# Kernel tuning notes

Hardware: AMD Instinct MI355X
Metric: run time of the kernel (lower is better)

The kernel has to match this reference:

```python
import jax, jax.numpy as jnp
import numpy as np

LN_EPS = 1e-5


def setup_inputs() -> dict:
    key = jax.random.key(0)
    ks = jax.random.split(key, 5)
    N, E, D = 50000, 600000, 128
    x = jax.random.normal(ks[0], (N, D), dtype=jnp.float32)
    edge_index = jax.random.randint(ks[1], (2, E), 0, N, dtype=jnp.int64)
    W_l = jax.random.normal(ks[2], (D, D), dtype=jnp.float32) * (1.0 / np.sqrt(D))
    b_l = jnp.zeros((D,), dtype=jnp.float32)
    W_r = jax.random.normal(ks[3], (D, D), dtype=jnp.float32) * (1.0 / np.sqrt(D))
    gamma = jnp.ones((D,), dtype=jnp.float32)
    beta = jnp.zeros((D,), dtype=jnp.float32)
    return {"x": x, "edge_index": edge_index, "W_l": W_l, "b_l": b_l,
            "W_r": W_r, "gamma": gamma, "beta": beta}


def reference(x, edge_index, W_l, b_l, W_r, gamma, beta):
    # SAGEConv (mean aggregation): out = lin_l(mean_{j in N(i)} x_j) + lin_r(x_i)
    N = x.shape[0]
    src, dst = edge_index[0], edge_index[1]
    msg = x[src]                                                # (E, D) gather
    agg = jax.ops.segment_sum(msg, dst, num_segments=N)         # (N, D) scatter-add
    cnt = jax.ops.segment_sum(jnp.ones_like(dst, dtype=x.dtype), dst, num_segments=N)
    mean = agg / jnp.maximum(cnt, 1.0)[:, None]
    h = mean @ W_l.T + b_l + x @ W_r.T                          # (N, D)
    # LayerNorm over feature dim
    mu = jnp.mean(h, axis=-1, keepdims=True)
    var = jnp.mean(jnp.square(h - mu), axis=-1, keepdims=True)
    h = (h - mu) * jax.lax.rsqrt(var + LN_EPS) * gamma + beta
    # ReLU; Dropout is identity in eval mode
    return jax.nn.relu(h)
```

## Files before the change

### kernel.cpp

```cpp
#include <hip/hip_runtime.h>
#include <stdint.h>

#define DIM 128
#define LN_EPS 1e-5f
#define BROWS 32
#define BINB 256
#define NT1 1024
#define SCAP 8
#define NBKT_MAX 1600
#define LELLS 56
#define LOVF 64
#define OVFCAP 4096
#define ATS 264
#define PINIT ((int)0xAAAAAAAA)

typedef __attribute__((ext_vector_type(8))) short bf16x8;
typedef __attribute__((ext_vector_type(4))) float f32x4;

static __device__ __forceinline__ uint16_t f2bf(float f) {
    uint32_t u = __float_as_uint(f);
    return (uint16_t)((u + 0x7fffu + ((u >> 16) & 1u)) >> 16);
}
static __device__ __forceinline__ float bf_lo(uint32_t w) {
    return __uint_as_float(w << 16);
}
static __device__ __forceinline__ float bf_hi(uint32_t w) {
    return __uint_as_float(w & 0xffff0000u);
}

__global__ __launch_bounds__(NT1) void bin_kernel(
    const int* __restrict__ ei,
    const float* __restrict__ x,
    const float* __restrict__ Wl,
    const float* __restrict__ Wr,
    uint8_t* __restrict__ cnt, uint32_t* __restrict__ bedge,
    int* __restrict__ novf, int* __restrict__ ovf,
    uint16_t* __restrict__ x16, uint16_t* __restrict__ wc,
    int E, int N, int nbkt)
{
    __shared__ int hist[NBKT_MAX];
    const int t = threadIdx.x, b = blockIdx.x;

    for (int i = t; i < nbkt; i += NT1) hist[i] = 0;
    __syncthreads();

    const int chunk = (E + BINB - 1) / BINB;
    const int e0 = b * chunk;
    const int e1 = (e0 + chunk < E) ? e0 + chunk : E;

    for (int e = e0 + t; e < e1; e += NT1)
        atomicAdd(&hist[ei[E + e] >> 5], 1);
    __syncthreads();

    for (int i = t; i < nbkt; i += NT1) {
        int c = hist[i];
        cnt[(size_t)i * BINB + b] = (uint8_t)(c > 255 ? 255 : c);
        hist[i] = 0;
    }
    __syncthreads();

    for (int e = e0 + t; e < e1; e += NT1) {
        int src = ei[e];
        int dst = ei[E + e];
        int bkt = dst >> 5;
        int r = atomicAdd(&hist[bkt], 1);
        if (r < SCAP) {
            bedge[((size_t)bkt * BINB + b) * SCAP + r] =
                ((uint32_t)(dst & 31) << 27) | (uint32_t)src;
        } else {
            int q = atomicAdd(novf, 1) - PINIT;
            if (q >= 0 && q < OVFCAP) { ovf[2 * q] = dst; ovf[2 * q + 1] = src; }
        }
    }

    {
        int tid = b * NT1 + t, nth = BINB * NT1;
        int nxp = (N * DIM) >> 1;
        for (int i = tid; i < nxp; i += nth) {
            float2 v = *(const float2*)(x + 2 * i);
            uint32_t u = ((uint32_t)f2bf(v.y) << 16) | (uint32_t)f2bf(v.x);
            ((uint32_t*)x16)[i] = u;
        }
        for (int i = tid; i < DIM * 256; i += nth) {
            int d = i >> 8, k = i & 255;
            float v = (k < DIM) ? Wl[d * DIM + k] : Wr[d * DIM + (k - DIM)];
            wc[i] = f2bf(v);
        }
    }
}

__global__ __launch_bounds__(256, 4) void fused_kernel(
    const uint16_t* __restrict__ x16,
    const uint8_t* __restrict__ cnt,
    const uint32_t* __restrict__ bedge,
    const int* __restrict__ novf,
    const int* __restrict__ ovf,
    const uint16_t* __restrict__ wc,
    const float* __restrict__ bl,
    const float* __restrict__ gma,
    const float* __restrict__ bta,
    float* __restrict__ out,
    int N, int E)
{
    __shared__ int ell_s[BROWS][LELLS];
    __shared__ int cnt_s[BROWS];
    __shared__ int lovf_s[LOVF];
    __shared__ int nlovf_s;
    __shared__ uint16_t atile[2][16 * ATS];
    __shared__ float pln[2][16][2][2];

    const int t    = threadIdx.x;
    const int lane = t & 63;
    const int w    = t >> 6;
    const int p    = w >> 1;
    const int h    = w & 1;
    const int tile_row0 = blockIdx.x * BROWS + p * 16;
    const int grow0     = tile_row0 + h * 8;
    const int lb        = p * 16 + h * 8;

    if (t < BROWS) cnt_s[t] = 0;
    if (t == BROWS) nlovf_s = 0;
    __syncthreads();

    if (t < BINB) {
        int c = cnt[(size_t)blockIdx.x * BINB + t];
        c = (c < SCAP) ? c : SCAP;
        const uint32_t* sp = bedge + ((size_t)blockIdx.x * BINB + t) * SCAP;
        for (int r = 0; r < c; ++r) {
            uint32_t pk = sp[r];
            int local = pk >> 27;
            int rr = atomicAdd(&cnt_s[local], 1);
            if (rr < LELLS) ell_s[local][rr] = (int)(pk & 0x07FFFFFF);
            else {
                int q = atomicAdd(&nlovf_s, 1);
                if (q < LOVF) lovf_s[q] = (int)pk;
            }
        }
    }
    __syncthreads();

    int dgx[8], nell[8], mx = 0;
    #pragma unroll
    for (int r = 0; r < 8; ++r) {
        int d = __builtin_amdgcn_readfirstlane(cnt_s[lb + r]);
        dgx[r] = d;
        int tt = d < LELLS ? d : LELLS;
        nell[r] = tt;
        mx = (tt > mx) ? tt : mx;
    }

    int soff[8];
    #pragma unroll
    for (int r = 0; r < 8; ++r)
        soff[r] = (lane < nell[r]) ? (ell_s[lb + r][lane] << 8) : 0;

    float m0[8], m1[8];
    #pragma unroll
    for (int r = 0; r < 8; ++r) { m0[r] = 0.0f; m1[r] = 0.0f; }

    const char* xb = (const char*)x16;
    uint32_t u[8];
    #pragma unroll
    for (int r = 0; r < 8; ++r) {
        int o = __builtin_amdgcn_readlane(soff[r], 0);
        u[r] = *(const uint32_t*)(xb + (uint32_t)o + 4 * lane);
    }

    for (int j = 0; j < mx; ++j) {
        uint32_t un[8];
        int jn = (j + 1 < mx) ? j + 1 : j;
        #pragma unroll
        for (int r = 0; r < 8; ++r) {
            int o = __builtin_amdgcn_readlane(soff[r], jn);
            un[r] = *(const uint32_t*)(xb + (uint32_t)o + 4 * lane);
        }
        #pragma unroll
        for (int r = 0; r < 8; ++r) {
            float pr = (j < nell[r]) ? 1.0f : 0.0f;
            m0[r] = fmaf(pr, bf_lo(u[r]), m0[r]);
            m1[r] = fmaf(pr, bf_hi(u[r]), m1[r]);
            u[r] = un[r];
        }
    }

    {
        int nl = __builtin_amdgcn_readfirstlane(nlovf_s);
        nl = (nl < 0) ? 0 : (nl > LOVF ? LOVF : nl);
        for (int i = 0; i < nl; ++i) {
            uint32_t pk = (uint32_t)lovf_s[i];
            int local = pk >> 27;
            if (local >= lb && local < lb + 8) {
                int srco = (int)(pk & 0x07FFFFFF);
                uint32_t uu = *(const uint32_t*)(x16 + (size_t)srco * DIM + 2 * lane);
                float v0 = bf_lo(uu), v1 = bf_hi(uu);
                #pragma unroll
                for (int r = 0; r < 8; ++r) {
                    float pr = (local == lb + r) ? 1.0f : 0.0f;
                    m0[r] = fmaf(pr, v0, m0[r]);
                    m1[r] = fmaf(pr, v1, m1[r]);
                }
            }
        }
    }

    {
        int no = __builtin_amdgcn_readfirstlane(novf[0]) - PINIT;
        no = (no < 0) ? 0 : (no > OVFCAP ? OVFCAP : no);
        for (int i = 0; i < no; ++i) {
            int dsto = __builtin_amdgcn_readfirstlane(ovf[2 * i]);
            int srco = __builtin_amdgcn_readfirstlane(ovf[2 * i + 1]);
            if (dsto >= grow0 && dsto < grow0 + 8) {
                uint32_t uu = *(const uint32_t*)(x16 + (size_t)srco * DIM + 2 * lane);
                float v0 = bf_lo(uu), v1 = bf_hi(uu);
                #pragma unroll
                for (int r = 0; r < 8; ++r) {
                    bool hit = (dsto == grow0 + r);
                    float pr = hit ? 1.0f : 0.0f;
                    m0[r] = fmaf(pr, v0, m0[r]);
                    m1[r] = fmaf(pr, v1, m1[r]);
                    dgx[r] += hit ? 1 : 0;
                }
            }
        }
    }

    {
        uint16_t* at = atile[p];
        #pragma unroll
        for (int r = 0; r < 8; ++r) {
            int row = grow0 + r;
            int rr = (row < N) ? row : 0;
            float rc = (dgx[r] > 0) ? (1.0f / (float)dgx[r]) : 0.0f;
            int lr = h * 8 + r;
            ushort2 mu2;
            mu2.x = f2bf(m0[r] * rc);
            mu2.y = f2bf(m1[r] * rc);
            *(ushort2*)&at[lr * ATS + 2 * lane] = mu2;
            uint32_t xv = *(const uint32_t*)(x16 + (size_t)rr * DIM + 2 * lane);
            *(uint32_t*)&at[lr * ATS + 128 + 2 * lane] = xv;
        }
    }
    __syncthreads();

    const int nsub = lane & 15;
    const int quad = lane >> 4;
    const uint16_t* at = atile[p];

    f32x4 acc[4];
    #pragma unroll
    for (int tt = 0; tt < 4; ++tt) {
        float b = bl[(h * 4 + tt) * 16 + nsub];
        acc[tt] = (f32x4){b, b, b, b};
    }

    #pragma unroll
    for (int c = 0; c < 8; ++c) {
        bf16x8 af = *(const bf16x8*)&at[nsub * ATS + c * 32 + quad * 8];
        #pragma unroll
        for (int tt = 0; tt < 4; ++tt) {
            int tg = h * 4 + tt;
            bf16x8 bfr = *(const bf16x8*)&wc[(size_t)(tg * 16 + nsub) * 256 + c * 32 + quad * 8];
            acc[tt] = __builtin_amdgcn_mfma_f32_16x16x32_bf16(af, bfr, acc[tt], 0, 0, 0);
        }
    }

    #pragma unroll
    for (int i = 0; i < 4; ++i) {
        float s = 0.0f, q = 0.0f;
        #pragma unroll
        for (int tt = 0; tt < 4; ++tt) {
            float v = acc[tt][i];
            s += v;
            q += v * v;
        }
        #pragma unroll
        for (int off = 1; off < 16; off <<= 1) {
            s += __shfl_xor(s, off, 64);
            q += __shfl_xor(q, off, 64);
        }
        if (nsub == 0) {
            pln[p][quad * 4 + i][h][0] = s;
            pln[p][quad * 4 + i][h][1] = q;
        }
    }
    __syncthreads();

    #pragma unroll
    for (int i = 0; i < 4; ++i) {
        int lrow = quad * 4 + i;
        float s = pln[p][lrow][0][0] + pln[p][lrow][1][0];
        float q = pln[p][lrow][0][1] + pln[p][lrow][1][1];
        float mu = s * (1.0f / 128.0f);
        float var = q * (1.0f / 128.0f) - mu * mu;
        float rs = rsqrtf(fmaxf(var, 0.0f) + LN_EPS);
        int grow = tile_row0 + lrow;
        if (grow < N) {
            float* op = out + (size_t)grow * DIM;
            #pragma unroll
            for (int tt = 0; tt < 4; ++tt) {
                int f = (h * 4 + tt) * 16 + nsub;
                float o = fmaxf((acc[tt][i] - mu) * rs * gma[f] + bta[f], 0.0f);
                op[f] = o;
            }
        }
    }
}

extern "C" void kernel_launch(void* const* d_in, const int* in_sizes, int n_in,
                              void* d_out, int out_size, void* d_ws, size_t ws_size,
                              hipStream_t stream) {
    const float* x  = (const float*)d_in[0];
    const int* ei   = (const int*)d_in[1];
    const float* Wl = (const float*)d_in[2];
    const float* bl = (const float*)d_in[3];
    const float* Wr = (const float*)d_in[4];
    const float* ga = (const float*)d_in[5];
    const float* be = (const float*)d_in[6];
    float* out = (float*)d_out;

    int N = in_sizes[0] / DIM;
    int E = in_sizes[1] / 2;
    int nbkt = (N + BROWS - 1) / BROWS;

    uint8_t* cnt    = (uint8_t*)d_ws;
    int* novf       = (int*)(cnt + (size_t)nbkt * BINB);
    uint16_t* wc    = (uint16_t*)(novf + 16);
    uint16_t* x16   = wc + DIM * 256;
    uint32_t* bedge = (uint32_t*)(x16 + (size_t)N * DIM);
    int* ovf        = (int*)(bedge + (size_t)nbkt * BINB * SCAP);

    bin_kernel<<<BINB, NT1, 0, stream>>>(
        ei, x, Wl, Wr, cnt, bedge, novf, ovf, x16, wc, E, N, nbkt);

    fused_kernel<<<nbkt, 256, 0, stream>>>(
        x16, cnt, bedge, novf, ovf, wc, bl, ga, be, out, N, E);
}
```

Baseline: 168.0 us.

## Gather neighbor rows with 16-byte loads, 4 rows per wave, software-pipelined

Reorganizes the mean-aggregation gather so each wave handles rows in 16-lane groups. Each lane issues dwordx4 loads covering 8 bf16 features, and 4 destination rows are gathered concurrently per instruction instead of one 256-byte row per wave-wide load. The loads are issued through inline asm and double-buffered with explicit vmcnt waits, so the next neighbor's fetch overlaps accumulation of the current one. The aim is fewer, wider memory instructions and more memory-level parallelism. In exchange it relies on hand-managed waitcnt and inline asm, and each lane keeps per-row neighbor counts instead of wave-uniform ones.

```diff
diff --git a/kernel.cpp b/kernel.cpp
--- a/kernel.cpp
+++ b/kernel.cpp
@@ -16,6 +16,7 @@
 
 typedef __attribute__((ext_vector_type(8))) short bf16x8;
 typedef __attribute__((ext_vector_type(4))) float f32x4;
+typedef __attribute__((ext_vector_type(4))) uint32_t u32x4;
 
 static __device__ __forceinline__ uint16_t f2bf(float f) {
     uint32_t u = __float_as_uint(f);
@@ -27,6 +28,12 @@
 static __device__ __forceinline__ float bf_hi(uint32_t w) {
     return __uint_as_float(w & 0xffff0000u);
 }
+
+#define CONS(Q, PR, A) do { float _p = (PR); \
+    A[0] = fmaf(_p, bf_lo(Q[0]), A[0]); A[1] = fmaf(_p, bf_hi(Q[0]), A[1]); \
+    A[2] = fmaf(_p, bf_lo(Q[1]), A[2]); A[3] = fmaf(_p, bf_hi(Q[1]), A[3]); \
+    A[4] = fmaf(_p, bf_lo(Q[2]), A[4]); A[5] = fmaf(_p, bf_hi(Q[2]), A[5]); \
+    A[6] = fmaf(_p, bf_lo(Q[3]), A[6]); A[7] = fmaf(_p, bf_hi(Q[3]), A[7]); } while (0)
 
 __global__ __launch_bounds__(NT1) void bin_kernel(
     const int* __restrict__ ei,
@@ -106,7 +113,7 @@
     __shared__ int cnt_s[BROWS];
     __shared__ int lovf_s[LOVF];
     __shared__ int nlovf_s;
-    __shared__ uint16_t atile[2][16 * ATS];
+    __shared__ __align__(16) uint16_t atile[2][16 * ATS];
     __shared__ float pln[2][16][2][2];
 
     const int t    = threadIdx.x;
@@ -122,7 +129,7 @@
     if (t == BROWS) nlovf_s = 0;
     __syncthreads();
 
-    if (t < BINB) {
+    {
         int c = cnt[(size_t)blockIdx.x * BINB + t];
         c = (c < SCAP) ? c : SCAP;
         const uint32_t* sp = bedge + ((size_t)blockIdx.x * BINB + t) * SCAP;
@@ -139,48 +146,67 @@
     }
     __syncthreads();
 
-    int dgx[8], nell[8], mx = 0;
+    const int rr4 = lane >> 4;
+    const int dq  = lane & 15;
+    const uint32_t dqo = (uint32_t)dq * 16u;
+    const int r0l = lb + rr4;
+    const int r1l = lb + 4 + rr4;
+    int dg0 = cnt_s[r0l];
+    int dg1 = cnt_s[r1l];
+    const int nl0 = dg0 < LELLS ? dg0 : LELLS;
+    const int nl1 = dg1 < LELLS ? dg1 : LELLS;
+
+    int mx = 0;
     #pragma unroll
     for (int r = 0; r < 8; ++r) {
         int d = __builtin_amdgcn_readfirstlane(cnt_s[lb + r]);
-        dgx[r] = d;
         int tt = d < LELLS ? d : LELLS;
-        nell[r] = tt;
         mx = (tt > mx) ? tt : mx;
     }
 
-    int soff[8];
-    #pragma unroll
-    for (int r = 0; r < 8; ++r)
-        soff[r] = (lane < nell[r]) ? (ell_s[lb + r][lane] << 8) : 0;
-
-    float m0[8], m1[8];
-    #pragma unroll
-    for (int r = 0; r < 8; ++r) { m0[r] = 0.0f; m1[r] = 0.0f; }
-
-    const char* xb = (const char*)x16;
-    uint32_t u[8];
-    #pragma unroll
-    for (int r = 0; r < 8; ++r) {
-        int o = __builtin_amdgcn_readlane(soff[r], 0);
-        u[r] = *(const uint32_t*)(xb + (uint32_t)o + 4 * lane);
-    }
-
-    for (int j = 0; j < mx; ++j) {
-        uint32_t un[8];
-        int jn = (j + 1 < mx) ? j + 1 : j;
-        #pragma unroll
-        for (int r = 0; r < 8; ++r) {
-            int o = __builtin_amdgcn_readlane(soff[r], jn);
-            un[r] = *(const uint32_t*)(xb + (uint32_t)o + 4 * lane);
-        }
-        #pragma unroll
-        for (int r = 0; r < 8; ++r) {
-            float pr = (j < nell[r]) ? 1.0f : 0.0f;
-            m0[r] = fmaf(pr, bf_lo(u[r]), m0[r]);
-            m1[r] = fmaf(pr, bf_hi(u[r]), m1[r]);
-            u[r] = un[r];
-        }
+    float a0[8], a1[8];
+    #pragma unroll
+    for (int k = 0; k < 8; ++k) { a0[k] = 0.0f; a1[k] = 0.0f; }
+
+    const uint64_t xb64 = (uint64_t)(uintptr_t)x16;
+    const int* rl0 = ell_s[r0l];
+    const int* rl1 = ell_s[r1l];
+
+    auto fetch = [&](int jj, int nl, const int* rowlist) -> uint32_t {
+        int slot = (jj < nl) ? jj : 0;
+        uint32_t v = (uint32_t)rowlist[slot];
+        return (jj < nl) ? ((v << 8) | dqo) : dqo;
+    };
+
+#define GLD4(dst, vo) \
+    asm volatile("global_load_dwordx4 %0, %1, %2 sc0" \
+                 : "=&v"(dst) : "v"(vo), "s"(xb64))
+
+    u32x4 qA0, qA1, qB0, qB1;
+    if (mx > 0) {
+        uint32_t vo0 = fetch(0, nl0, rl0);
+        uint32_t vo1 = fetch(0, nl1, rl1);
+        GLD4(qA0, vo0); GLD4(qA1, vo1);
+        for (int j = 0; j < mx; j += 2) {
+            int jb = j + 1;
+            vo0 = fetch(jb, nl0, rl0); vo1 = fetch(jb, nl1, rl1);
+            GLD4(qB0, vo0); GLD4(qB1, vo1);
+            asm volatile("s_waitcnt vmcnt(2)" ::: "memory");
+            __builtin_amdgcn_sched_barrier(0);
+            CONS(qA0, (j < nl0) ? 1.0f : 0.0f, a0);
+            CONS(qA1, (j < nl1) ? 1.0f : 0.0f, a1);
+            int jc = j + 2;
+            vo0 = fetch(jc, nl0, rl0); vo1 = fetch(jc, nl1, rl1);
+            GLD4(qA0, vo0); GLD4(qA1, vo1);
+            asm volatile("s_waitcnt vmcnt(2)" ::: "memory");
+            __builtin_amdgcn_sched_barrier(0);
+            if (jb < mx) {
+                CONS(qB0, (jb < nl0) ? 1.0f : 0.0f, a0);
+                CONS(qB1, (jb < nl1) ? 1.0f : 0.0f, a1);
+            }
+        }
+        asm volatile("s_waitcnt vmcnt(0)" ::: "memory");
+        __builtin_amdgcn_sched_barrier(0);
     }
 
     {
@@ -191,14 +217,9 @@
             int local = pk >> 27;
             if (local >= lb && local < lb + 8) {
                 int srco = (int)(pk & 0x07FFFFFF);
-                uint32_t uu = *(const uint32_t*)(x16 + (size_t)srco * DIM + 2 * lane);
-                float v0 = bf_lo(uu), v1 = bf_hi(uu);
-                #pragma unroll
-                for (int r = 0; r < 8; ++r) {
-                    float pr = (local == lb + r) ? 1.0f : 0.0f;
-                    m0[r] = fmaf(pr, v0, m0[r]);
-                    m1[r] = fmaf(pr, v1, m1[r]);
-                }
+                u32x4 qq = *(const u32x4*)(x16 + (size_t)srco * DIM + 8 * dq);
+                CONS(qq, (local == r0l) ? 1.0f : 0.0f, a0);
+                CONS(qq, (local == r1l) ? 1.0f : 0.0f, a1);
             }
         }
     }
@@ -210,35 +231,36 @@
             int dsto = __builtin_amdgcn_readfirstlane(ovf[2 * i]);
             int srco = __builtin_amdgcn_readfirstlane(ovf[2 * i + 1]);
             if (dsto >= grow0 && dsto < grow0 + 8) {
-                uint32_t uu = *(const uint32_t*)(x16 + (size_t)srco * DIM + 2 * lane);
-                float v0 = bf_lo(uu), v1 = bf_hi(uu);
-                #pragma unroll
-                for (int r = 0; r < 8; ++r) {
-                    bool hit = (dsto == grow0 + r);
-                    float pr = hit ? 1.0f : 0.0f;
-                    m0[r] = fmaf(pr, v0, m0[r]);
-                    m1[r] = fmaf(pr, v1, m1[r]);
-                    dgx[r] += hit ? 1 : 0;
-                }
+                u32x4 qq = *(const u32x4*)(x16 + (size_t)srco * DIM + 8 * dq);
+                int h0 = (dsto == grow0 + rr4) ? 1 : 0;
+                int h1 = (dsto == grow0 + 4 + rr4) ? 1 : 0;
+                CONS(qq, h0 ? 1.0f : 0.0f, a0);
+                CONS(qq, h1 ? 1.0f : 0.0f, a1);
+                dg0 += h0; dg1 += h1;
             }
         }
     }
 
     {
         uint16_t* at = atile[p];
+        float rc0 = (dg0 > 0) ? (1.0f / (float)dg0) : 0.0f;
+        float rc1 = (dg1 > 0) ? (1.0f / (float)dg1) : 0.0f;
+        int lr0 = h * 8 + rr4;
+        int lr1 = h * 8 + 4 + rr4;
+        u32x4 w0, w1;
         #pragma unroll
-        for (int r = 0; r < 8; ++r) {
-            int row = grow0 + r;
-            int rr = (row < N) ? row : 0;
-            float rc = (dgx[r] > 0) ? (1.0f / (float)dgx[r]) : 0.0f;
-            int lr = h * 8 + r;
-            ushort2 mu2;
-            mu2.x = f2bf(m0[r] * rc);
-            mu2.y = f2bf(m1[r] * rc);
-            *(ushort2*)&at[lr * ATS + 2 * lane] = mu2;
-            uint32_t xv = *(const uint32_t*)(x16 + (size_t)rr * DIM + 2 * lane);
-            *(uint32_t*)&at[lr * ATS + 128 + 2 * lane] = xv;
-        }
+        for (int i = 0; i < 4; ++i) {
+            w0[i] = ((uint32_t)f2bf(a0[2 * i + 1] * rc0) << 16) | f2bf(a0[2 * i] * rc0);
+            w1[i] = ((uint32_t)f2bf(a1[2 * i + 1] * rc1) << 16) | f2bf(a1[2 * i] * rc1);
+        }
+        *(u32x4*)&at[lr0 * ATS + 8 * dq] = w0;
+        *(u32x4*)&at[lr1 * ATS + 8 * dq] = w1;
+        int row0g = grow0 + rr4;     int rs0 = (row0g < N) ? row0g : 0;
+        int row1g = grow0 + 4 + rr4; int rs1 = (row1g < N) ? row1g : 0;
+        u32x4 xv0 = *(const u32x4*)(x16 + (size_t)rs0 * DIM + 8 * dq);
+        u32x4 xv1 = *(const u32x4*)(x16 + (size_t)rs1 * DIM + 8 * dq);
+        *(u32x4*)&at[lr0 * ATS + 128 + 8 * dq] = xv0;
+        *(u32x4*)&at[lr1 * ATS + 128 + 8 * dq] = xv1;
     }
     __syncthreads();
 
```

Result: faster. 156.9 us (-6.6%).
